# Kernel optimization log

Measured on AMD Instinct MI355X. Metric: run time of the kernel, lower is better.

## Reference

```python
import jax, jax.numpy as jnp
import numpy as np

N, E, D_IN, D_HID, D_OUT = 50000, 600000, 128, 128, 64


def setup_inputs() -> dict:
    key = jax.random.key(0)
    ks = jax.random.split(key, 8)
    x = jax.random.normal(ks[0], (N, D_IN), dtype=jnp.float32)
    edge_index = jax.random.randint(ks[1], (2, E), 0, N, dtype=jnp.int64)
    def glorot(k, fan_in, fan_out):
        s = (6.0 / (fan_in + fan_out)) ** 0.5
        return jax.random.uniform(k, (fan_in, fan_out), jnp.float32, -s, s)
    return {
        "x": x,
        "W1": glorot(ks[2], D_IN, D_HID), "b1": jnp.zeros((D_HID,), jnp.float32),
        "W2": glorot(ks[3], D_HID, D_HID), "b2": jnp.zeros((D_HID,), jnp.float32),
        "W3": glorot(ks[4], D_HID, D_OUT), "b3": jnp.zeros((D_OUT,), jnp.float32),
        "edge_index": edge_index,
    }


def reference(x, W1, b1, W2, b2, W3, b3, edge_index):
    n = x.shape[0]
    # GCN with self-loops: A_hat = A + I, norm = D^-1/2 A_hat D^-1/2
    loops = jnp.arange(n, dtype=edge_index.dtype)
    row = jnp.concatenate([edge_index[0], loops])  # source nodes
    col = jnp.concatenate([edge_index[1], loops])  # target nodes
    deg = jax.ops.segment_sum(jnp.ones_like(col, dtype=x.dtype), col, num_segments=n)
    dinv = jnp.where(deg > 0, jax.lax.rsqrt(deg), 0.0)
    norm = dinv[row] * dinv[col]  # [E+N]

    def gcn_conv(h, W, b):
        hw = h @ W                                   # [N, out]
        msg = hw[row] * norm[:, None]                # [E+N, out] gather + scale
        return jax.ops.segment_sum(msg, col, num_segments=n) + b

    h = jax.nn.relu(gcn_conv(x, W1, b1))
    h = jax.nn.relu(gcn_conv(h, W2, b2))
    return gcn_conv(h, W3, b3)
```

## Files before the change

### kernel.cpp

```cpp
#include <hip/hip_runtime.h>
#include <hip/hip_bf16.h>
#include <hip/hip_fp16.h>


typedef _Float16 h2 __attribute__((ext_vector_type(2)));
typedef _Float16 h8 __attribute__((ext_vector_type(8)));

__device__ inline float4 h4_to_f4(float2 raw) {
    __half2 lo = *reinterpret_cast<__half2*>(&raw.x);
    __half2 hi = *reinterpret_cast<__half2*>(&raw.y);
    float2 a = __half22float2(lo);
    float2 b = __half22float2(hi);
    return make_float4(a.x, a.y, b.x, b.y);
}

__device__ inline uint pack_h2(float a, float b) {
    __half2 h = __floats2half2_rn(a, b);
    return *reinterpret_cast<uint*>(&h);
}

__global__ __launch_bounds__(256) void zero_counts_kernel(int4* __restrict__ p, int n4) {
    int i = blockIdx.x * 256 + threadIdx.x;
    if (i < n4) p[i] = make_int4(0, 0, 0, 0);
}

__global__ __launch_bounds__(256) void f32_to_f16_kernel(const float4* __restrict__ in,
                                                         uint2* __restrict__ out, int n4) {
    int i = blockIdx.x * 256 + threadIdx.x;
    if (i < n4) {
        float4 v = in[i];
        out[i] = make_uint2(pack_h2(v.x, v.y), pack_h2(v.z, v.w));
    }
}

__global__ void count_edges_kernel(const int* __restrict__ col, int* __restrict__ counts, int E) {
    int e = blockIdx.x * blockDim.x + threadIdx.x;
    if (e < E) atomicAdd(&counts[col[e]], 1);
}

__global__ __launch_bounds__(256) void block_sum_kernel(const int* __restrict__ counts,
                                                        int* __restrict__ blocksum, int n) {
    int i = blockIdx.x * 256 + threadIdx.x;
    int v = (i < n) ? counts[i] : 0;
    #pragma unroll
    for (int d = 1; d < 64; d <<= 1) v += __shfl_xor(v, d);
    __shared__ int ws[4];
    if ((threadIdx.x & 63) == 0) ws[threadIdx.x >> 6] = v;
    __syncthreads();
    if (threadIdx.x == 0) blocksum[blockIdx.x] = ws[0] + ws[1] + ws[2] + ws[3];
}

__global__ __launch_bounds__(256) void scan_sums_kernel(const int* __restrict__ blocksum,
                                                        int* __restrict__ blockoff,
                                                        int* __restrict__ offsets, int nb, int n) {
    int tid = threadIdx.x;
    int lane = tid & 63, wid = tid >> 6;
    int orig = (tid < nb) ? blocksum[tid] : 0;
    int v = orig;
    #pragma unroll
    for (int d = 1; d < 64; d <<= 1) {
        int u = __shfl_up(v, d);
        if (lane >= d) v += u;
    }
    __shared__ int ws[4];
    if (lane == 63) ws[wid] = v;
    __syncthreads();
    int add = 0;
    for (int w = 0; w < wid; ++w) add += ws[w];
    v += add;
    if (tid < nb) blockoff[tid] = v - orig;
    if (tid == 255) offsets[n] = v;
}

__global__ __launch_bounds__(256) void write_offsets_kernel(const int* __restrict__ counts,
                                                            const int* __restrict__ blockoff,
                                                            int* __restrict__ offsets,
                                                            int* __restrict__ cursor,
                                                            float* __restrict__ dinv, int n) {
    int tid = threadIdx.x;
    int i = blockIdx.x * 256 + tid;
    int lane = tid & 63, wid = tid >> 6;
    int c = (i < n) ? counts[i] : 0;
    int v = c;
    #pragma unroll
    for (int d = 1; d < 64; d <<= 1) {
        int u = __shfl_up(v, d);
        if (lane >= d) v += u;
    }
    __shared__ int ws[4];
    if (lane == 63) ws[wid] = v;
    __syncthreads();
    int add = 0;
    for (int w = 0; w < wid; ++w) add += ws[w];
    int incl = v + add;
    if (i < n) {
        offsets[i] = blockoff[blockIdx.x] + incl - c;
        cursor[i] = 0;
        dinv[i] = rsqrtf((float)(c + 1));
    }
}

__global__ void fill_csr_kernel(const int* __restrict__ row, const int* __restrict__ col,
                                const int* __restrict__ offsets, int* __restrict__ cursor,
                                int* __restrict__ srcs, int E) {
    int e = blockIdx.x * blockDim.x + threadIdx.x;
    if (e < E) {
        int c = col[e];
        int pos = offsets[c] + atomicAdd(&cursor[c], 1);
        srcs[pos] = row[e];
    }
}

template <int DO>
__global__ __launch_bounds__(256, 2) void gemm16_kernel(const __half* __restrict__ A,
                                                        const float* __restrict__ W,
                                                        const float* __restrict__ dinv,
                                                        __half* __restrict__ out, int n) {
    constexpr int K = 128;
    constexpr int COLTH = DO / 8;
    constexpr int ROWTH = 256 / COLTH;
    constexpr int R = (DO == 128) ? 8 : 4;
    constexpr int BR = ROWTH * R;
    constexpr int HALF = DO / 2;

    __shared__ alignas(16) h2 Wl[(K / 2) * DO];

    int tid = threadIdx.x;
    for (int idx = tid; idx < (K / 2) * (DO / 4); idx += 256) {
        int k2 = idx / (DO / 4);
        int c4 = idx % (DO / 4);
        float4 w0 = ((const float4*)(W + (size_t)(2 * k2) * DO))[c4];
        float4 w1 = ((const float4*)(W + (size_t)(2 * k2 + 1) * DO))[c4];
        h2* dst = &Wl[k2 * DO + c4 * 4];
        h2 d0; d0.x = (_Float16)w0.x; d0.y = (_Float16)w1.x; dst[0] = d0;
        h2 d1; d1.x = (_Float16)w0.y; d1.y = (_Float16)w1.y; dst[1] = d1;
        h2 d2; d2.x = (_Float16)w0.z; d2.y = (_Float16)w1.z; dst[2] = d2;
        h2 d3; d3.x = (_Float16)w0.w; d3.y = (_Float16)w1.w; dst[3] = d3;
    }
    __syncthreads();

    int ct = tid % COLTH;
    int rt = tid / COLTH;
    int rb = blockIdx.x * BR + rt * R;

    int rowc[R];
    #pragma unroll
    for (int i = 0; i < R; ++i) {
        int row = rb + i;
        rowc[i] = (row < n) ? row : (n - 1);
    }

    float acc[R][8];
    #pragma unroll
    for (int i = 0; i < R; ++i)
        #pragma unroll
        for (int c = 0; c < 8; ++c) acc[i][c] = 0.f;

    #pragma unroll 2
    for (int k8 = 0; k8 < K / 8; ++k8) {
        h8 av[R];
        #pragma unroll
        for (int i = 0; i < R; ++i) {
            av[i] = ((const h8*)(A + (size_t)rowc[i] * K))[k8];
        }
        #pragma unroll
        for (int kk = 0; kk < 4; ++kk) {
            int k2 = k8 * 4 + kk;
            h2 w0[4], w1[4];
            *(uint4*)w0 = *(const uint4*)(&Wl[k2 * DO + ct * 4]);
            *(uint4*)w1 = *(const uint4*)(&Wl[k2 * DO + HALF + ct * 4]);
            #pragma unroll
            for (int i = 0; i < R; ++i) {
                h2 a; a.x = av[i][2 * kk]; a.y = av[i][2 * kk + 1];
                #pragma unroll
                for (int c = 0; c < 4; ++c) {
                    acc[i][c]     = __builtin_amdgcn_fdot2(a, w0[c], acc[i][c], false);
                    acc[i][4 + c] = __builtin_amdgcn_fdot2(a, w1[c], acc[i][4 + c], false);
                }
            }
        }
    }

    #pragma unroll
    for (int i = 0; i < R; ++i) {
        int row = rb + i;
        if (row < n) {
            float dv = dinv[row];
            uint2 q0 = make_uint2(pack_h2(acc[i][0] * dv, acc[i][1] * dv),
                                  pack_h2(acc[i][2] * dv, acc[i][3] * dv));
            uint2 q1 = make_uint2(pack_h2(acc[i][4] * dv, acc[i][5] * dv),
                                  pack_h2(acc[i][6] * dv, acc[i][7] * dv));
            *(uint2*)(out + (size_t)row * DO + ct * 4) = q0;
            *(uint2*)(out + (size_t)row * DO + HALF + ct * 4) = q1;
        }
    }
}

template <int DO, bool RELU, bool F16OUT>
__global__ __launch_bounds__(256) void agg_kernel(const __half* __restrict__ hw,
                                                  const int* __restrict__ offsets,
                                                  const int* __restrict__ srcs,
                                                  const float* __restrict__ dinv,
                                                  const float* __restrict__ bias,
                                                  void* __restrict__ outp, int n) {
    constexpr int TPD = DO / 4;
    constexpr int DPB = 256 / TPD;
    int d = blockIdx.x * DPB + threadIdx.x / TPD;
    int j = threadIdx.x % TPD;
    if (d >= n) return;

    const float2* hw2 = (const float2*)hw;
    int beg = offsets[d];
    int end = offsets[d + 1];

    float4 acc = h4_to_f4(hw2[(size_t)d * TPD + j]);

    int e = beg;
    for (; e + 8 <= end; e += 8) {
        int s0 = srcs[e + 0], s1 = srcs[e + 1], s2 = srcs[e + 2], s3 = srcs[e + 3];
        int s4 = srcs[e + 4], s5 = srcs[e + 5], s6 = srcs[e + 6], s7 = srcs[e + 7];
        float4 v0 = h4_to_f4(hw2[(size_t)s0 * TPD + j]);
        float4 v1 = h4_to_f4(hw2[(size_t)s1 * TPD + j]);
        float4 v2 = h4_to_f4(hw2[(size_t)s2 * TPD + j]);
        float4 v3 = h4_to_f4(hw2[(size_t)s3 * TPD + j]);
        float4 v4 = h4_to_f4(hw2[(size_t)s4 * TPD + j]);
        float4 v5 = h4_to_f4(hw2[(size_t)s5 * TPD + j]);
        float4 v6 = h4_to_f4(hw2[(size_t)s6 * TPD + j]);
        float4 v7 = h4_to_f4(hw2[(size_t)s7 * TPD + j]);
        acc.x += v0.x; acc.y += v0.y; acc.z += v0.z; acc.w += v0.w;
        acc.x += v1.x; acc.y += v1.y; acc.z += v1.z; acc.w += v1.w;
        acc.x += v2.x; acc.y += v2.y; acc.z += v2.z; acc.w += v2.w;
        acc.x += v3.x; acc.y += v3.y; acc.z += v3.z; acc.w += v3.w;
        acc.x += v4.x; acc.y += v4.y; acc.z += v4.z; acc.w += v4.w;
        acc.x += v5.x; acc.y += v5.y; acc.z += v5.z; acc.w += v5.w;
        acc.x += v6.x; acc.y += v6.y; acc.z += v6.z; acc.w += v6.w;
        acc.x += v7.x; acc.y += v7.y; acc.z += v7.z; acc.w += v7.w;
    }
    for (; e + 4 <= end; e += 4) {
        int s0 = srcs[e + 0], s1 = srcs[e + 1], s2 = srcs[e + 2], s3 = srcs[e + 3];
        float4 v0 = h4_to_f4(hw2[(size_t)s0 * TPD + j]);
        float4 v1 = h4_to_f4(hw2[(size_t)s1 * TPD + j]);
        float4 v2 = h4_to_f4(hw2[(size_t)s2 * TPD + j]);
        float4 v3 = h4_to_f4(hw2[(size_t)s3 * TPD + j]);
        acc.x += v0.x; acc.y += v0.y; acc.z += v0.z; acc.w += v0.w;
        acc.x += v1.x; acc.y += v1.y; acc.z += v1.z; acc.w += v1.w;
        acc.x += v2.x; acc.y += v2.y; acc.z += v2.z; acc.w += v2.w;
        acc.x += v3.x; acc.y += v3.y; acc.z += v3.z; acc.w += v3.w;
    }
    for (; e < end; ++e) {
        float4 v = h4_to_f4(hw2[(size_t)srcs[e] * TPD + j]);
        acc.x += v.x; acc.y += v.y; acc.z += v.z; acc.w += v.w;
    }

    float di = dinv[d];
    float4 b4 = ((const float4*)bias)[j];
    acc.x = b4.x + di * acc.x;
    acc.y = b4.y + di * acc.y;
    acc.z = b4.z + di * acc.z;
    acc.w = b4.w + di * acc.w;

    if (RELU) {
        acc.x = fmaxf(acc.x, 0.f); acc.y = fmaxf(acc.y, 0.f);
        acc.z = fmaxf(acc.z, 0.f); acc.w = fmaxf(acc.w, 0.f);
    }
    if (F16OUT) {
        uint2 q = make_uint2(pack_h2(acc.x, acc.y), pack_h2(acc.z, acc.w));
        ((uint2*)outp)[(size_t)d * TPD + j] = q;
    } else {
        ((float4*)outp)[(size_t)d * TPD + j] = acc;
    }
}

extern "C" void kernel_launch(void* const* d_in, const int* in_sizes, int n_in,
                              void* d_out, int out_size, void* d_ws, size_t ws_size,
                              hipStream_t stream) {
    const float* x  = (const float*)d_in[0];
    const float* W1 = (const float*)d_in[1];
    const float* b1 = (const float*)d_in[2];
    const float* W2 = (const float*)d_in[3];
    const float* b2 = (const float*)d_in[4];
    const float* W3 = (const float*)d_in[5];
    const float* b3 = (const float*)d_in[6];
    const int*   ei = (const int*)d_in[7];

    const int N = in_sizes[0] / 128;
    const int E = in_sizes[7] / 2;
    const int* rowi = ei;
    const int* coli = ei + E;

    float* out = (float*)d_out;

    char* ws = (char*)d_ws;
    size_t off = 0;
    auto alloc = [&](size_t bytes) -> void* {
        void* p = ws + off;
        off = (off + bytes + 255) & ~(size_t)255;
        return p;
    };
    const int NB = (N + 255) / 256;
    float* dinv     = (float*)alloc((size_t)N * 4);
    int*   counts   = (int*)  alloc(((size_t)N + 4) * 4);
    int*   offsets  = (int*)  alloc((size_t)(N + 1) * 4);
    int*   cursor   = (int*)  alloc((size_t)N * 4);
    int*   blocksum = (int*)  alloc((size_t)NB * 4);
    int*   blockoff = (int*)  alloc((size_t)NB * 4);
    int*   srcs     = (int*)  alloc((size_t)E * 4);
    __half* x16     = (__half*)alloc((size_t)N * 128 * 2);
    __half* hw16    = (__half*)alloc((size_t)N * 128 * 2);
    __half* h16     = (__half*)alloc((size_t)N * 128 * 2);

    const int n4 = (N + 3) / 4;
    zero_counts_kernel<<<(n4 + 255) / 256, 256, 0, stream>>>((int4*)counts, n4);
    count_edges_kernel<<<(E + 255) / 256, 256, 0, stream>>>(coli, counts, E);
    block_sum_kernel<<<NB, 256, 0, stream>>>(counts, blocksum, N);
    scan_sums_kernel<<<1, 256, 0, stream>>>(blocksum, blockoff, offsets, NB, N);
    write_offsets_kernel<<<NB, 256, 0, stream>>>(counts, blockoff, offsets, cursor, dinv, N);
    fill_csr_kernel<<<(E + 255) / 256, 256, 0, stream>>>(rowi, coli, offsets, cursor, srcs, E);
    const int xc4 = N * 128 / 4;
    f32_to_f16_kernel<<<(xc4 + 255) / 256, 256, 0, stream>>>((const float4*)x, (uint2*)x16, xc4);

    gemm16_kernel<128><<<(N + 127) / 128, 256, 0, stream>>>(x16, W1, dinv, hw16, N);
    agg_kernel<128, true, true><<<(N + 7) / 8, 256, 0, stream>>>(hw16, offsets, srcs, dinv, b1, h16, N);

    gemm16_kernel<128><<<(N + 127) / 128, 256, 0, stream>>>(h16, W2, dinv, hw16, N);
    agg_kernel<128, true, true><<<(N + 7) / 8, 256, 0, stream>>>(hw16, offsets, srcs, dinv, b2, h16, N);

    gemm16_kernel<64><<<(N + 127) / 128, 256, 0, stream>>>(h16, W3, dinv, hw16, N);
    agg_kernel<64, false, false><<<(N + 15) / 16, 256, 0, stream>>>(hw16, offsets, srcs, dinv, b3, out, N);
}
```

Baseline: 223.5 us.

## Fuse f32-to-f16 input conversion into first GEMM; one wavefront per node aggregation

Removes the separate x-to-fp16 conversion kernel and its buffer by letting the first GEMM read fp32 rows and pack them to fp16 in registers. This saves one launch and a round trip of the fp16 copy of x, at the cost of twice the bytes per A load in that GEMM. The aggregation kernel is also remapped so each 64-lane wavefront owns one destination node, with each lane handling 2 halves (D=128) or 1 half (D=64). The narrower per-lane loads may lower per-lane memory-level parallelism, and the D=64 path now does 2-byte gathers.

```diff
diff --git a/kernel.cpp b/kernel.cpp
--- a/kernel.cpp
+++ b/kernel.cpp
@@ -6,31 +6,29 @@
 typedef _Float16 h2 __attribute__((ext_vector_type(2)));
 typedef _Float16 h8 __attribute__((ext_vector_type(8)));
 
-__device__ inline float4 h4_to_f4(float2 raw) {
-    __half2 lo = *reinterpret_cast<__half2*>(&raw.x);
-    __half2 hi = *reinterpret_cast<__half2*>(&raw.y);
-    float2 a = __half22float2(lo);
-    float2 b = __half22float2(hi);
-    return make_float4(a.x, a.y, b.x, b.y);
-}
-
 __device__ inline uint pack_h2(float a, float b) {
     __half2 h = __floats2half2_rn(a, b);
     return *reinterpret_cast<uint*>(&h);
 }
 
+__device__ inline h2 pack_h2v(float a, float b) {
+    uint u = pack_h2(a, b);
+    return *reinterpret_cast<h2*>(&u);
+}
+
+__device__ inline float2 u_to_f2(uint u) {
+    __half2 h = *reinterpret_cast<__half2*>(&u);
+    return __half22float2(h);
+}
+
+__device__ inline float us_to_f(unsigned short u) {
+    __half h = *reinterpret_cast<__half*>(&u);
+    return __half2float(h);
+}
+
 __global__ __launch_bounds__(256) void zero_counts_kernel(int4* __restrict__ p, int n4) {
     int i = blockIdx.x * 256 + threadIdx.x;
     if (i < n4) p[i] = make_int4(0, 0, 0, 0);
-}
-
-__global__ __launch_bounds__(256) void f32_to_f16_kernel(const float4* __restrict__ in,
-                                                         uint2* __restrict__ out, int n4) {
-    int i = blockIdx.x * 256 + threadIdx.x;
-    if (i < n4) {
-        float4 v = in[i];
-        out[i] = make_uint2(pack_h2(v.x, v.y), pack_h2(v.z, v.w));
-    }
 }
 
 __global__ void count_edges_kernel(const int* __restrict__ col, int* __restrict__ counts, int E) {
@@ -111,8 +109,8 @@
     }
 }
 
-template <int DO>
-__global__ __launch_bounds__(256, 2) void gemm16_kernel(const __half* __restrict__ A,
+template <int DO, bool AF32>
+__global__ __launch_bounds__(256, 2) void gemm16_kernel(const void* __restrict__ Ap,
                                                         const float* __restrict__ W,
                                                         const float* __restrict__ dinv,
                                                         __half* __restrict__ out, int n) {
@@ -161,7 +159,22 @@
         h8 av[R];
         #pragma unroll
         for (int i = 0; i < R; ++i) {
-            av[i] = ((const h8*)(A + (size_t)rowc[i] * K))[k8];
+            if (AF32) {
+                const float4* A4 = (const float4*)Ap;
+                float4 lo = A4[(size_t)rowc[i] * (K / 4) + k8 * 2];
+                float4 hi = A4[(size_t)rowc[i] * (K / 4) + k8 * 2 + 1];
+                h2 t0 = pack_h2v(lo.x, lo.y);
+                h2 t1 = pack_h2v(lo.z, lo.w);
+                h2 t2 = pack_h2v(hi.x, hi.y);
+                h2 t3 = pack_h2v(hi.z, hi.w);
+                h8 a;
+                a[0] = t0.x; a[1] = t0.y; a[2] = t1.x; a[3] = t1.y;
+                a[4] = t2.x; a[5] = t2.y; a[6] = t3.x; a[7] = t3.y;
+                av[i] = a;
+            } else {
+                const h8* A8 = (const h8*)Ap;
+                av[i] = A8[(size_t)rowc[i] * (K / 8) + k8];
+            }
         }
         #pragma unroll
         for (int kk = 0; kk < 4; ++kk) {
@@ -203,71 +216,88 @@
                                                   const float* __restrict__ dinv,
                                                   const float* __restrict__ bias,
                                                   void* __restrict__ outp, int n) {
-    constexpr int TPD = DO / 4;
-    constexpr int DPB = 256 / TPD;
-    int d = blockIdx.x * DPB + threadIdx.x / TPD;
-    int j = threadIdx.x % TPD;
+    int wid = threadIdx.x >> 6;
+    int lane = threadIdx.x & 63;
+    int d = blockIdx.x * 4 + wid;
     if (d >= n) return;
 
-    const float2* hw2 = (const float2*)hw;
     int beg = offsets[d];
     int end = offsets[d + 1];
-
-    float4 acc = h4_to_f4(hw2[(size_t)d * TPD + j]);
-
-    int e = beg;
-    for (; e + 8 <= end; e += 8) {
-        int s0 = srcs[e + 0], s1 = srcs[e + 1], s2 = srcs[e + 2], s3 = srcs[e + 3];
-        int s4 = srcs[e + 4], s5 = srcs[e + 5], s6 = srcs[e + 6], s7 = srcs[e + 7];
-        float4 v0 = h4_to_f4(hw2[(size_t)s0 * TPD + j]);
-        float4 v1 = h4_to_f4(hw2[(size_t)s1 * TPD + j]);
-        float4 v2 = h4_to_f4(hw2[(size_t)s2 * TPD + j]);
-        float4 v3 = h4_to_f4(hw2[(size_t)s3 * TPD + j]);
-        float4 v4 = h4_to_f4(hw2[(size_t)s4 * TPD + j]);
-        float4 v5 = h4_to_f4(hw2[(size_t)s5 * TPD + j]);
-        float4 v6 = h4_to_f4(hw2[(size_t)s6 * TPD + j]);
-        float4 v7 = h4_to_f4(hw2[(size_t)s7 * TPD + j]);
-        acc.x += v0.x; acc.y += v0.y; acc.z += v0.z; acc.w += v0.w;
-        acc.x += v1.x; acc.y += v1.y; acc.z += v1.z; acc.w += v1.w;
-        acc.x += v2.x; acc.y += v2.y; acc.z += v2.z; acc.w += v2.w;
-        acc.x += v3.x; acc.y += v3.y; acc.z += v3.z; acc.w += v3.w;
-        acc.x += v4.x; acc.y += v4.y; acc.z += v4.z; acc.w += v4.w;
-        acc.x += v5.x; acc.y += v5.y; acc.z += v5.z; acc.w += v5.w;
-        acc.x += v6.x; acc.y += v6.y; acc.z += v6.z; acc.w += v6.w;
-        acc.x += v7.x; acc.y += v7.y; acc.z += v7.z; acc.w += v7.w;
-    }
-    for (; e + 4 <= end; e += 4) {
-        int s0 = srcs[e + 0], s1 = srcs[e + 1], s2 = srcs[e + 2], s3 = srcs[e + 3];
-        float4 v0 = h4_to_f4(hw2[(size_t)s0 * TPD + j]);
-        float4 v1 = h4_to_f4(hw2[(size_t)s1 * TPD + j]);
-        float4 v2 = h4_to_f4(hw2[(size_t)s2 * TPD + j]);
-        float4 v3 = h4_to_f4(hw2[(size_t)s3 * TPD + j]);
-        acc.x += v0.x; acc.y += v0.y; acc.z += v0.z; acc.w += v0.w;
-        acc.x += v1.x; acc.y += v1.y; acc.z += v1.z; acc.w += v1.w;
-        acc.x += v2.x; acc.y += v2.y; acc.z += v2.z; acc.w += v2.w;
-        acc.x += v3.x; acc.y += v3.y; acc.z += v3.z; acc.w += v3.w;
-    }
-    for (; e < end; ++e) {
-        float4 v = h4_to_f4(hw2[(size_t)srcs[e] * TPD + j]);
-        acc.x += v.x; acc.y += v.y; acc.z += v.z; acc.w += v.w;
-    }
-
     float di = dinv[d];
-    float4 b4 = ((const float4*)bias)[j];
-    acc.x = b4.x + di * acc.x;
-    acc.y = b4.y + di * acc.y;
-    acc.z = b4.z + di * acc.z;
-    acc.w = b4.w + di * acc.w;
-
-    if (RELU) {
-        acc.x = fmaxf(acc.x, 0.f); acc.y = fmaxf(acc.y, 0.f);
-        acc.z = fmaxf(acc.z, 0.f); acc.w = fmaxf(acc.w, 0.f);
-    }
-    if (F16OUT) {
-        uint2 q = make_uint2(pack_h2(acc.x, acc.y), pack_h2(acc.z, acc.w));
-        ((uint2*)outp)[(size_t)d * TPD + j] = q;
+
+    if constexpr (DO == 128) {
+        const uint* hwu = (const uint*)hw;
+        size_t base = (size_t)d * 64 + lane;
+        float2 acc = u_to_f2(hwu[base]);
+
+        int e = beg;
+        for (; e + 8 <= end; e += 8) {
+            int s0 = srcs[e + 0], s1 = srcs[e + 1], s2 = srcs[e + 2], s3 = srcs[e + 3];
+            int s4 = srcs[e + 4], s5 = srcs[e + 5], s6 = srcs[e + 6], s7 = srcs[e + 7];
+            uint v0 = hwu[(size_t)s0 * 64 + lane];
+            uint v1 = hwu[(size_t)s1 * 64 + lane];
+            uint v2 = hwu[(size_t)s2 * 64 + lane];
+            uint v3 = hwu[(size_t)s3 * 64 + lane];
+            uint v4 = hwu[(size_t)s4 * 64 + lane];
+            uint v5 = hwu[(size_t)s5 * 64 + lane];
+            uint v6 = hwu[(size_t)s6 * 64 + lane];
+            uint v7 = hwu[(size_t)s7 * 64 + lane];
+            float2 f0 = u_to_f2(v0), f1 = u_to_f2(v1), f2 = u_to_f2(v2), f3 = u_to_f2(v3);
+            float2 f4 = u_to_f2(v4), f5 = u_to_f2(v5), f6 = u_to_f2(v6), f7 = u_to_f2(v7);
+            acc.x += f0.x; acc.y += f0.y; acc.x += f1.x; acc.y += f1.y;
+            acc.x += f2.x; acc.y += f2.y; acc.x += f3.x; acc.y += f3.y;
+            acc.x += f4.x; acc.y += f4.y; acc.x += f5.x; acc.y += f5.y;
+            acc.x += f6.x; acc.y += f6.y; acc.x += f7.x; acc.y += f7.y;
+        }
+        for (; e + 4 <= end; e += 4) {
+            int s0 = srcs[e + 0], s1 = srcs[e + 1], s2 = srcs[e + 2], s3 = srcs[e + 3];
+            float2 f0 = u_to_f2(hwu[(size_t)s0 * 64 + lane]);
+            float2 f1 = u_to_f2(hwu[(size_t)s1 * 64 + lane]);
+            float2 f2 = u_to_f2(hwu[(size_t)s2 * 64 + lane]);
+            float2 f3 = u_to_f2(hwu[(size_t)s3 * 64 + lane]);
+            acc.x += f0.x; acc.y += f0.y; acc.x += f1.x; acc.y += f1.y;
+            acc.x += f2.x; acc.y += f2.y; acc.x += f3.x; acc.y += f3.y;
+        }
+        for (; e < end; ++e) {
+            float2 f = u_to_f2(hwu[(size_t)srcs[e] * 64 + lane]);
+            acc.x += f.x; acc.y += f.y;
+        }
+
+        float2 b2 = ((const float2*)bias)[lane];
+        acc.x = b2.x + di * acc.x;
+        acc.y = b2.y + di * acc.y;
+        if (RELU) { acc.x = fmaxf(acc.x, 0.f); acc.y = fmaxf(acc.y, 0.f); }
+        if (F16OUT) {
+            ((uint*)outp)[base] = pack_h2(acc.x, acc.y);
+        } else {
+            ((float2*)outp)[base] = acc;
+        }
     } else {
-        ((float4*)outp)[(size_t)d * TPD + j] = acc;
+        const unsigned short* hwu = (const unsigned short*)hw;
+        size_t base = (size_t)d * 64 + lane;
+        float acc = us_to_f(hwu[base]);
+
+        int e = beg;
+        for (; e + 8 <= end; e += 8) {
+            int s0 = srcs[e + 0], s1 = srcs[e + 1], s2 = srcs[e + 2], s3 = srcs[e + 3];
+            int s4 = srcs[e + 4], s5 = srcs[e + 5], s6 = srcs[e + 6], s7 = srcs[e + 7];
+            float f0 = us_to_f(hwu[(size_t)s0 * 64 + lane]);
+            float f1 = us_to_f(hwu[(size_t)s1 * 64 + lane]);
+            float f2 = us_to_f(hwu[(size_t)s2 * 64 + lane]);
+            float f3 = us_to_f(hwu[(size_t)s3 * 64 + lane]);
+            float f4 = us_to_f(hwu[(size_t)s4 * 64 + lane]);
+            float f5 = us_to_f(hwu[(size_t)s5 * 64 + lane]);
+            float f6 = us_to_f(hwu[(size_t)s6 * 64 + lane]);
+            float f7 = us_to_f(hwu[(size_t)s7 * 64 + lane]);
+            acc += f0 + f1 + f2 + f3 + f4 + f5 + f6 + f7;
+        }
+        for (; e < end; ++e) {
+            acc += us_to_f(hwu[(size_t)srcs[e] * 64 + lane]);
+        }
+
+        acc = bias[lane] + di * acc;
+        if (RELU) acc = fmaxf(acc, 0.f);
+        ((float*)outp)[base] = acc;
     }
 }
 
@@ -305,7 +335,6 @@
     int*   blocksum = (int*)  alloc((size_t)NB * 4);
     int*   blockoff = (int*)  alloc((size_t)NB * 4);
     int*   srcs     = (int*)  alloc((size_t)E * 4);
-    __half* x16     = (__half*)alloc((size_t)N * 128 * 2);
     __half* hw16    = (__half*)alloc((size_t)N * 128 * 2);
     __half* h16     = (__half*)alloc((size_t)N * 128 * 2);
 
@@ -316,15 +345,13 @@
     scan_sums_kernel<<<1, 256, 0, stream>>>(blocksum, blockoff, offsets, NB, N);
     write_offsets_kernel<<<NB, 256, 0, stream>>>(counts, blockoff, offsets, cursor, dinv, N);
     fill_csr_kernel<<<(E + 255) / 256, 256, 0, stream>>>(rowi, coli, offsets, cursor, srcs, E);
-    const int xc4 = N * 128 / 4;
-    f32_to_f16_kernel<<<(xc4 + 255) / 256, 256, 0, stream>>>((const float4*)x, (uint2*)x16, xc4);
-
-    gemm16_kernel<128><<<(N + 127) / 128, 256, 0, stream>>>(x16, W1, dinv, hw16, N);
-    agg_kernel<128, true, true><<<(N + 7) / 8, 256, 0, stream>>>(hw16, offsets, srcs, dinv, b1, h16, N);
-
-    gemm16_kernel<128><<<(N + 127) / 128, 256, 0, stream>>>(h16, W2, dinv, hw16, N);
-    agg_kernel<128, true, true><<<(N + 7) / 8, 256, 0, stream>>>(hw16, offsets, srcs, dinv, b2, h16, N);
-
-    gemm16_kernel<64><<<(N + 127) / 128, 256, 0, stream>>>(h16, W3, dinv, hw16, N);
-    agg_kernel<64, false, false><<<(N + 15) / 16, 256, 0, stream>>>(hw16, offsets, srcs, dinv, b3, out, N);
-}
+
+    gemm16_kernel<128, true><<<(N + 127) / 128, 256, 0, stream>>>(x, W1, dinv, hw16, N);
+    agg_kernel<128, true, true><<<(N + 3) / 4, 256, 0, stream>>>(hw16, offsets, srcs, dinv, b1, h16, N);
+
+    gemm16_kernel<128, false><<<(N + 127) / 128, 256, 0, stream>>>(h16, W2, dinv, hw16, N);
+    agg_kernel<128, true, true><<<(N + 3) / 4, 256, 0, stream>>>(hw16, offsets, srcs, dinv, b2, h16, N);
+
+    gemm16_kernel<64, false><<<(N + 127) / 128, 256, 0, stream>>>(h16, W3, dinv, hw16, N);
+    agg_kernel<64, false, false><<<(N + 3) / 4, 256, 0, stream>>>(hw16, offsets, srcs, dinv, b3, out, N);
+}
```

Result: slower. 242.9 us (+8.7%).
